# Kernel tuning notes

Measured on AMD Instinct MI355X. Metric: run time of the kernel, lower is better.

Reference implementation:

```python
import jax, jax.numpy as jnp
import numpy as np

HEADS = 8
LANDMARKS = 256
PINV_ITERS = 6
CONV_K = 33


def _layernorm(x, g, b, eps=1e-5):
    mu = x.mean(-1, keepdims=True)
    var = x.var(-1, keepdims=True)
    return (x - mu) * jax.lax.rsqrt(var + eps) * g + b


def _pinv(x, iters=PINV_ITERS):
    # Moore-Penrose iterative pseudo-inverse (lucidrains nystrom-attention)
    ax = jnp.abs(x)
    denom = ax.sum(-1).max() * ax.sum(-2).max()  # global max, as in torch.max()
    z = jnp.swapaxes(x, -1, -2) / denom
    I = jnp.eye(x.shape[-1], dtype=x.dtype)
    for _ in range(iters):
        xz = x @ z
        z = 0.25 * z @ (13 * I - xz @ (15 * I - xz @ (7 * I - xz)))
    return z


def _nystrom_attn(x, qkv_w, out_w, out_b, conv_w):
    b, n, dim = x.shape
    h, m = HEADS, LANDMARKS
    dh = dim // h
    pad = (-n) % m  # pad at the FRONT so n divisible by num_landmarks
    xp = jnp.pad(x, ((0, 0), (pad, 0), (0, 0)))
    npad = n + pad
    qkv = xp @ qkv_w  # [b, npad, 3*dim]
    q, k, v = jnp.split(qkv, 3, axis=-1)

    def to_heads(t):
        return t.reshape(b, npad, h, dh).transpose(0, 2, 1, 3)  # [b,h,npad,dh]

    q, k, v = to_heads(q), to_heads(k), to_heads(v)
    q = q * (dh ** -0.5)
    l = npad // m  # tokens per landmark
    q_l = q.reshape(b, h, m, l, dh).mean(3)  # landmark means [b,h,m,dh]
    k_l = k.reshape(b, h, m, l, dh).mean(3)
    a1 = jax.nn.softmax(jnp.einsum('bhid,bhjd->bhij', q, k_l), axis=-1)   # [b,h,npad,m]
    a2 = jax.nn.softmax(jnp.einsum('bhid,bhjd->bhij', q_l, k_l), axis=-1)  # [b,h,m,m]
    a3 = jax.nn.softmax(jnp.einsum('bhid,bhjd->bhij', q_l, k), axis=-1)   # [b,h,m,npad]
    out = (a1 @ _pinv(a2)) @ (a3 @ v)  # [b,h,npad,dh]
    # residual depthwise conv over sequence dim, one channel per head (bias=False)
    res = jax.lax.conv_general_dilated(
        v, conv_w, window_strides=(1, 1),
        padding=((CONV_K // 2, CONV_K // 2), (0, 0)),
        dimension_numbers=('NCHW', 'OIHW', 'NCHW'),
        feature_group_count=HEADS)
    out = out + res
    out = out.transpose(0, 2, 1, 3).reshape(b, npad, dim)
    out = out @ out_w + out_b
    return out[:, -n:]  # drop front padding


def setup_inputs():
    key = jax.random.key(0)
    ks = jax.random.split(key, 16)
    D_IN, D, C = 1024, 512, 2
    return {
        'feats': jax.random.normal(ks[0], (2, 8000, D_IN), jnp.float32),
        'fc1_w': jax.random.normal(ks[1], (D_IN, D), jnp.float32) * 0.02,
        'fc1_b': jnp.zeros((D,), jnp.float32),
        'cls_token': jax.random.normal(ks[2], (1, 1, D), jnp.float32),
        'ln1_g': jnp.ones((D,), jnp.float32),
        'ln1_b': jnp.zeros((D,), jnp.float32),
        'qkv1_w': jax.random.normal(ks[3], (D, 3 * D), jnp.float32) * 0.02,
        'out1_w': jax.random.normal(ks[4], (D, D), jnp.float32) * 0.02,
        'out1_b': jnp.zeros((D,), jnp.float32),
        'conv1_w': jax.random.normal(ks[5], (HEADS, 1, CONV_K, 1), jnp.float32) * 0.02,
        'ln2_g': jnp.ones((D,), jnp.float32),
        'ln2_b': jnp.zeros((D,), jnp.float32),
        'qkv2_w': jax.random.normal(ks[6], (D, 3 * D), jnp.float32) * 0.02,
        'out2_w': jax.random.normal(ks[7], (D, D), jnp.float32) * 0.02,
        'out2_b': jnp.zeros((D,), jnp.float32),
        'conv2_w': jax.random.normal(ks[8], (HEADS, 1, CONV_K, 1), jnp.float32) * 0.02,
        'normf_g': jnp.ones((D,), jnp.float32),
        'normf_b': jnp.zeros((D,), jnp.float32),
        'fc2_w': jax.random.normal(ks[9], (D, C), jnp.float32) * 0.02,
        'fc2_b': jnp.zeros((C,), jnp.float32),
    }


def reference(feats, fc1_w, fc1_b, cls_token, ln1_g, ln1_b, qkv1_w, out1_w, out1_b, conv1_w,
              ln2_g, ln2_b, qkv2_w, out2_w, out2_b, conv2_w, normf_g, normf_b, fc2_w, fc2_b):
    h = jax.nn.relu(feats @ fc1_w + fc1_b)  # [B,N,512]
    B = h.shape[0]
    cls = jnp.broadcast_to(cls_token, (B, 1, cls_token.shape[-1]))
    h = jnp.concatenate([cls, h], axis=1)  # [B,N+1,512]
    h = h + _nystrom_attn(_layernorm(h, ln1_g, ln1_b), qkv1_w, out1_w, out1_b, conv1_w)
    h = h + _nystrom_attn(_layernorm(h, ln2_g, ln2_b), qkv2_w, out2_w, out2_b, conv2_w)
    h_cls = _layernorm(h, normf_g, normf_b)[:, 0]
    logits = h_cls @ fc2_w + fc2_b
    y_prob = jax.nn.softmax(logits, axis=1)
    y_hat = jnp.argmax(logits, axis=1)
    return logits, y_prob, y_hat
```

## Files before the change

kernel.cpp:

```cpp
#include <hip/hip_runtime.h>

typedef unsigned short u16;
typedef __attribute__((ext_vector_type(8))) short short8;
typedef __attribute__((ext_vector_type(4))) float f32x4;

__device__ __forceinline__ float bf2f(u16 x){
  union { unsigned u; float f; } c; c.u = ((unsigned)x) << 16; return c.f;
}
__device__ __forceinline__ u16 f2bf(float f){
  union { float f; unsigned u; } c; c.f = f;
  unsigned u = c.u;
  return (u16)((u + 0x7FFFu + ((u >> 16) & 1u)) >> 16);
}
__device__ __forceinline__ unsigned pk2(float a, float b){
  return (unsigned)f2bf(a) | ((unsigned)f2bf(b) << 16);
}
__device__ __forceinline__ void hilo(float v, u16& hi, u16& lo){
  hi = f2bf(v); lo = f2bf(v - bf2f(hi));
}

__device__ __forceinline__ void gload16(const void* g, void* l){
  __builtin_amdgcn_global_load_lds(
    (const __attribute__((address_space(1))) void*)g,
    (__attribute__((address_space(3))) void*)l, 16, 0, 0);
}

__global__ void k_cls(const float* cls, float* h){
  int b = blockIdx.x, t = threadIdx.x;
  for (int c=t; c<512; c+=256)
    h[((long)b*8192+191)*512 + c] = cls[c];
}

__global__ void k_cvtT(const float* Wm, u16* wT, int K, int N){
  __shared__ float tile[32][33];
  int n0 = blockIdx.x*32, k0 = blockIdx.y*32;
  int x = threadIdx.x & 31, y = threadIdx.x >> 5;
  #pragma unroll
  for (int p=0;p<4;p++) tile[y+8*p][x] = Wm[(long)(k0+y+8*p)*N + n0 + x];
  __syncthreads();
  #pragma unroll
  for (int p=0;p<4;p++) wT[(long)(n0+y+8*p)*K + k0 + x] = f2bf(tile[x][y+8*p]);
}

template<int MODE>
__launch_bounds__(256)
__global__ void k_gemm(const void* Av, const u16* Bt, const float* bias,
                       float* hout, u16* qo, u16* ko, u16* vo,
                       int M, int N, int K){
  __shared__ __align__(16) u16 As[128*32];
  __shared__ __align__(16) u16 Bs[128*32];
  const int tid = threadIdx.x;
  const int wave = tid>>6, lane = tid&63;
  const int m0 = blockIdx.x*128, n0 = blockIdx.y*128;
  const int wr = wave>>1, wc = wave&1;
  f32x4 acc[4][4];
  #pragma unroll
  for (int i=0;i<4;i++)
    #pragma unroll
    for (int j=0;j<4;j++) acc[i][j] = (f32x4){0.f,0.f,0.f,0.f};

  for (int k0=0; k0<K; k0+=32){
    if constexpr (MODE == 0){
      int r = tid>>1, half = tid&1;
      const float* gp = (const float*)Av + (long)(m0+r)*K + k0 + half*16;
      float4 f0 = *(const float4*)(gp+0);
      float4 f1 = *(const float4*)(gp+4);
      float4 f2 = *(const float4*)(gp+8);
      float4 f3 = *(const float4*)(gp+12);
      uint4 pa, pb;
      pa.x = pk2(f0.x,f0.y); pa.y = pk2(f0.z,f0.w);
      pa.z = pk2(f1.x,f1.y); pa.w = pk2(f1.z,f1.w);
      pb.x = pk2(f2.x,f2.y); pb.y = pk2(f2.z,f2.w);
      pb.z = pk2(f3.x,f3.y); pb.w = pk2(f3.z,f3.w);
      uint4* dst = (uint4*)&As[r*32 + half*16];
      dst[0] = pa; dst[1] = pb;
    } else {
      #pragma unroll
      for (int ci=0; ci<2; ++ci){
        int c = wave*2 + ci;
        int r = (c<<4) + (lane>>2), kq = lane&3;
        const u16* gp;
        if constexpr (MODE == 1){
          gp = (const u16*)Av + (long)(m0+r)*K + k0 + kq*8;
        } else {
          int rr = m0 + r; int b = rr>>13, pos = rr&8191;
          int cc = k0 + kq*8; int hh = cc>>6, d = cc&63;
          gp = (const u16*)Av + ((long)(b*8+hh)*8192 + pos)*64 + d;
        }
        gload16(gp, &As[c*512]);
      }
    }
    #pragma unroll
    for (int ci=0; ci<2; ++ci){
      int c = wave*2 + ci;
      int r = (c<<4) + (lane>>2), kq = lane&3;
      gload16(Bt + (long)(n0+r)*K + k0 + kq*8, &Bs[c*512]);
    }
    __syncthreads();
    short8 af[4], bf[4];
    int arow = wr*64 + (lane&15);
    int brow = wc*64 + (lane&15);
    int koff = (lane>>4)*8;
    #pragma unroll
    for (int i=0;i<4;i++){
      af[i] = *(const short8*)&As[(arow + i*16)*32 + koff];
      bf[i] = *(const short8*)&Bs[(brow + i*16)*32 + koff];
    }
    #pragma unroll
    for (int i=0;i<4;i++)
      #pragma unroll
      for (int j=0;j<4;j++)
        acc[i][j] = __builtin_amdgcn_mfma_f32_16x16x32_bf16(bf[j], af[i], acc[i][j], 0,0,0);
    __syncthreads();
  }

  const int lc = lane&15, hi4 = (lane>>4)*4;
  if constexpr (MODE == 0){
    #pragma unroll
    for (int j=0;j<4;j++){
      int cb = n0 + wc*64 + j*16 + hi4;
      float4 bb = *(const float4*)&bias[cb];
      #pragma unroll
      for (int i=0;i<4;i++){
        int row = m0 + wr*64 + i*16 + lc;
        int b = (row >= 8000) ? 1 : 0;
        int tok = row - b*8000;
        float4 o;
        o.x = fmaxf(acc[i][j][0] + bb.x, 0.f);
        o.y = fmaxf(acc[i][j][1] + bb.y, 0.f);
        o.z = fmaxf(acc[i][j][2] + bb.z, 0.f);
        o.w = fmaxf(acc[i][j][3] + bb.w, 0.f);
        *(float4*)&hout[((long)(b*8192 + 192 + tok))*512 + cb] = o;
      }
    }
  } else if constexpr (MODE == 1){
    #pragma unroll
    for (int j=0;j<4;j++){
      int cb = n0 + wc*64 + j*16 + hi4;
      int which = cb>>9, head = (cb>>6)&7, d = cb&63;
      u16* base = (which==0) ? qo : (which==1 ? ko : vo);
      float scale = (which==0) ? 0.125f : 1.0f;
      #pragma unroll
      for (int i=0;i<4;i++){
        int row = m0 + wr*64 + i*16 + lc;
        int b = row>>13, pos = row&8191;
        unsigned o2[2];
        o2[0] = pk2(acc[i][j][0]*scale, acc[i][j][1]*scale);
        o2[1] = pk2(acc[i][j][2]*scale, acc[i][j][3]*scale);
        *(uint2*)&base[((long)(b*8+head)*8192 + pos)*64 + d] = *(uint2*)o2;
      }
    }
  } else {
    #pragma unroll
    for (int j=0;j<4;j++){
      int cb = n0 + wc*64 + j*16 + hi4;
      float4 bb = *(const float4*)&bias[cb];
      #pragma unroll
      for (int i=0;i<4;i++){
        int row = m0 + wr*64 + i*16 + lc;
        int pos = row&8191;
        if (pos < 191) continue;
        float4* p = (float4*)&hout[(long)row*512 + cb];
        float4 cur = *p;
        cur.x += acc[i][j][0] + bb.x;
        cur.y += acc[i][j][1] + bb.y;
        cur.z += acc[i][j][2] + bb.z;
        cur.w += acc[i][j][3] + bb.w;
        *p = cur;
      }
    }
  }
}

__global__ void k_ln(const float* hsrc, const float* g, const float* bt, u16* xlnb){
  int row = blockIdx.x;
  int pos = row & 8191;
  int t = threadIdx.x;
  long base = (long)row*512 + t*2;
  if (pos < 191){ *(unsigned*)&xlnb[base] = 0u; return; }
  float2 x = *(const float2*)(hsrc + base);
  __shared__ float red[4];
  float s = x.x + x.y;
  for (int off=32; off; off>>=1) s += __shfl_down(s, off, 64);
  if ((t&63)==0) red[t>>6]=s;
  __syncthreads();
  float mean = (red[0]+red[1]+red[2]+red[3]) * (1.f/512.f);
  __syncthreads();
  float d0 = x.x-mean, d1 = x.y-mean;
  float ss = d0*d0 + d1*d1;
  for (int off=32; off; off>>=1) ss += __shfl_down(ss, off, 64);
  if ((t&63)==0) red[t>>6]=ss;
  __syncthreads();
  float rstd = rsqrtf((red[0]+red[1]+red[2]+red[3])*(1.f/512.f) + 1e-5f);
  float o0 = d0*rstd*g[t*2]   + bt[t*2];
  float o1 = d1*rstd*g[t*2+1] + bt[t*2+1];
  *(unsigned*)&xlnb[base] = pk2(o0, o1);
}

__global__ void k_landmark(const u16* src, float* dst, u16* dstb){
  int g = blockIdx.x, bh = blockIdx.y, d = threadIdx.x;
  const u16* p = src + (((long)bh*8192) + g*32)*64 + d;
  float s = 0.f;
  #pragma unroll
  for (int j=0;j<32;j++) s += bf2f(p[j*64]);
  s *= (1.f/32.f);
  long o = ((long)bh*256 + g)*64 + d;
  dst[o] = s;
  dstb[o] = f2bf(s);
}

__launch_bounds__(256)
__global__ void k_a2(const float* qlm, const float* klm, float* a2, u16* a2Nh, u16* a2Nl){
  __shared__ float qls[16][68];
  __shared__ float kls[64][65];
  __shared__ float Sf[16][260];
  __shared__ float red[4];
  int bh = blockIdx.y, rt = blockIdx.x, t = threadIdx.x;
  const float* qp = qlm + ((long)bh*256 + rt*16)*64;
  { int fidx = t*4; int r = fidx>>6, c = fidx&63;
    float4 a = *(const float4*)(qp + fidx);
    qls[r][c]=a.x; qls[r][c+1]=a.y; qls[r][c+2]=a.z; qls[r][c+3]=a.w; }
  const float* kp = klm + (long)bh*16384;
  int cl = t & 63, ig = t >> 6;
  for (int kt=0; kt<4; ++kt){
    __syncthreads();
    for (int l=0;l<4;l++){
      int fidx = (l*256+t)*4; int r = fidx>>6, c = fidx&63;
      float4 a = *(const float4*)(kp + (long)(kt*64+r)*64 + c);
      kls[r][c]=a.x; kls[r][c+1]=a.y; kls[r][c+2]=a.z; kls[r][c+3]=a.w;
    }
    __syncthreads();
    float s0=0,s1=0,s2=0,s3=0;
    #pragma unroll
    for (int d=0;d<64;d++){
      float kv = kls[cl][d];
      s0 += qls[ig*4+0][d]*kv;
      s1 += qls[ig*4+1][d]*kv;
      s2 += qls[ig*4+2][d]*kv;
      s3 += qls[ig*4+3][d]*kv;
    }
    Sf[ig*4+0][kt*64+cl]=s0;
    Sf[ig*4+1][kt*64+cl]=s1;
    Sf[ig*4+2][kt*64+cl]=s2;
    Sf[ig*4+3][kt*64+cl]=s3;
  }
  __syncthreads();
  long ab = ((long)bh*256 + rt*16)*256;
  for (int i=0;i<16;i++){
    float val = Sf[i][t];
    float m = val;
    for (int off=1; off<64; off<<=1) m = fmaxf(m, __shfl_xor(m,off,64));
    if ((t&63)==0) red[t>>6]=m;
    __syncthreads();
    m = fmaxf(fmaxf(red[0],red[1]),fmaxf(red[2],red[3]));
    __syncthreads();
    float e = __expf(val - m);
    float sum = e;
    for (int off=1; off<64; off<<=1) sum += __shfl_xor(sum,off,64);
    if ((t&63)==0) red[t>>6]=sum;
    __syncthreads();
    sum = red[0]+red[1]+red[2]+red[3];
    __syncthreads();
    float o = e/sum;
    long idx = ab + (long)i*256 + t;
    a2[idx] = o;
    u16 hi, lo; hilo(o, hi, lo);
    a2Nh[idx]=hi; a2Nl[idx]=lo;
  }
}

__global__ void k_colrow(const float* a2, float* rc){
  int bh = blockIdx.x, t = threadIdx.x;
  const float* p = a2 + (long)bh*65536;
  float cs=0.f, rs=0.f;
  for (int r=0;r<256;r++) cs += fabsf(p[(long)r*256 + t]);
  for (int c=0;c<256;c++) rs += fabsf(p[(long)t*256 + c]);
  __shared__ float red[4];
  for (int off=32; off; off>>=1) cs = fmaxf(cs, __shfl_down(cs,off,64));
  if ((t&63)==0) red[t>>6]=cs;
  __syncthreads();
  if (t==0) rc[bh] = fmaxf(fmaxf(red[0],red[1]),fmaxf(red[2],red[3]));
  __syncthreads();
  for (int off=32; off; off>>=1) rs = fmaxf(rs, __shfl_down(rs,off,64));
  if ((t&63)==0) red[t>>6]=rs;
  __syncthreads();
  if (t==0) rc[16+bh] = fmaxf(fmaxf(red[0],red[1]),fmaxf(red[2],red[3]));
}
__global__ void k_denom(const float* rc, float* denom){
  float cm=0.f, rm=0.f;
  for (int i=0;i<16;i++){ cm=fmaxf(cm,rc[i]); rm=fmaxf(rm,rc[16+i]); }
  *denom = cm*rm;
}

__global__ void k_z0p(const float* a2, const float* denom,
                      u16* zNh, u16* zNl, u16* zTh, u16* zTl){
  __shared__ float tile[32][33];
  int bh = blockIdx.z;
  int c0 = blockIdx.x*32, r0 = blockIdx.y*32;
  int x = threadIdx.x & 31, y = threadIdx.x >> 5;
  const float* p = a2 + (long)bh*65536;
  float inv = 1.0f / (*denom);
  long zb = (long)bh*65536;
  #pragma unroll
  for (int yy=0; yy<32; yy+=8){
    float vv = p[(long)(r0+y+yy)*256 + c0 + x];
    tile[y+yy][x] = vv;
    float val = vv*inv;
    u16 hi, lo; hilo(val, hi, lo);
    long idx = zb + (long)(r0+y+yy)*256 + c0 + x;
    zTh[idx]=hi; zTl[idx]=lo;
  }
  __syncthreads();
  #pragma unroll
  for (int yy=0; yy<32; yy+=8){
    float val = tile[x][y+yy]*inv;
    u16 hi, lo; hilo(val, hi, lo);
    long idx = zb + (long)(c0+y+yy)*256 + r0 + x;
    zNh[idx]=hi; zNl[idx]=lo;
  }
}

struct NC {
  const u16 *Ah, *Al, *Bh, *Bl;
  const u16 *E1h, *E1l, *E2h, *E2l;
  u16 *oNh, *oNl, *oTh, *oTl, *oBF;
  long strA, strB, strO;
  float sa, s1, s2;
};

__launch_bounds__(64)
__global__ void k_nmm(NC c0, NC c1){
  int gz = blockIdx.z;
  int bh = gz & 15;
  NC C = (gz>>4) ? c1 : c0;
  __shared__ __align__(16) char smem[8192];
  u16* AsH = (u16*)smem;
  u16* AsL = (u16*)(smem + 2048);
  u16* BsH = (u16*)(smem + 4096);
  u16* BsL = (u16*)(smem + 6144);
  float* T = (float*)smem;
  int lane = threadIdx.x;
  int m0 = blockIdx.x*32, n0 = blockIdx.y*32;
  int lc = lane&15, hi = lane>>4;
  f32x4 acc[2][2];
  #pragma unroll
  for (int i=0;i<2;i++)
    #pragma unroll
    for (int j=0;j<2;j++) acc[i][j] = (f32x4){0.f,0.f,0.f,0.f};

  const u16* pAh = C.Ah + (long)bh*C.strA;
  const u16* pAl = C.Al + (long)bh*C.strA;
  const u16* pBh = C.Bh + (long)bh*C.strB;
  const u16* pBl = C.Bl + (long)bh*C.strB;
  int r0 = lane>>2, kq = lane&3;
  int r1 = r0 + 16;
  long offA0 = (long)(m0+r0)*256 + ((kq ^ ((r0>>1)&3))<<3);
  long offA1 = (long)(m0+r1)*256 + ((kq ^ ((r1>>1)&3))<<3);
  long offB0 = (long)(n0+r0)*256 + ((kq ^ ((r0>>1)&3))<<3);
  long offB1 = (long)(n0+r1)*256 + ((kq ^ ((r1>>1)&3))<<3);

  for (int k0=0; k0<256; k0+=32){
    gload16(pAh + offA0 + k0, smem + 0);
    gload16(pAh + offA1 + k0, smem + 1024);
    gload16(pAl + offA0 + k0, smem + 2048);
    gload16(pAl + offA1 + k0, smem + 3072);
    gload16(pBh + offB0 + k0, smem + 4096);
    gload16(pBh + offB1 + k0, smem + 5120);
    gload16(pBl + offB0 + k0, smem + 6144);
    gload16(pBl + offB1 + k0, smem + 7168);
    __syncthreads();
    short8 aH[2], aL[2], bH[2], bL[2];
    #pragma unroll
    for (int i=0;i<2;i++){
      int ra = i*16 + lc;
      int ca = ((hi ^ ((ra>>1)&3)))<<3;
      aH[i] = *(const short8*)&AsH[ra*32 + ca];
      aL[i] = *(const short8*)&AsL[ra*32 + ca];
      bH[i] = *(const short8*)&BsH[ra*32 + ca];
      bL[i] = *(const short8*)&BsL[ra*32 + ca];
    }
    #pragma unroll
    for (int i=0;i<2;i++)
      #pragma unroll
      for (int j=0;j<2;j++){
        acc[i][j] = __builtin_amdgcn_mfma_f32_16x16x32_bf16(aH[i], bH[j], acc[i][j], 0,0,0);
        acc[i][j] = __builtin_amdgcn_mfma_f32_16x16x32_bf16(aH[i], bL[j], acc[i][j], 0,0,0);
        acc[i][j] = __builtin_amdgcn_mfma_f32_16x16x32_bf16(aL[i], bH[j], acc[i][j], 0,0,0);
      }
    __syncthreads();
  }

  long eb = (long)bh*65536;
  #pragma unroll
  for (int i=0;i<2;i++)
    #pragma unroll
    for (int j=0;j<2;j++){
      int rg = i*16 + hi*4;
      int cg = j*16 + lc;
      #pragma unroll
      for (int r=0;r<4;r++){
        float val = C.sa*acc[i][j][r];
        long ei = eb + (long)(m0+rg+r)*256 + (n0+cg);
        if (C.E1h) val += C.s1*(bf2f(C.E1h[ei]) + bf2f(C.E1l[ei]));
        if (C.E2h) val += C.s2*(bf2f(C.E2h[ei]) + bf2f(C.E2l[ei]));
        T[(rg+r)*34 + cg] = val;
      }
    }
  __syncthreads();
  int rr = lane>>1, cc0 = (lane&1)*16;
  if (C.oBF){
    u16 tmp[16];
    #pragma unroll
    for (int m=0;m<16;m++) tmp[m] = f2bf(T[rr*34 + cc0 + m]);
    long ob = (long)bh*C.strO + (long)(m0+rr)*256 + n0 + cc0;
    *(uint4*)&C.oBF[ob]   = *(uint4*)&tmp[0];
    *(uint4*)&C.oBF[ob+8] = *(uint4*)&tmp[8];
  } else {
    u16 th[16], tl[16];
    #pragma unroll
    for (int m=0;m<16;m++) hilo(T[rr*34 + cc0 + m], th[m], tl[m]);
    long ob = (long)bh*65536 + (long)(m0+rr)*256 + n0 + cc0;
    *(uint4*)&C.oNh[ob]   = *(uint4*)&th[0];
    *(uint4*)&C.oNh[ob+8] = *(uint4*)&th[8];
    *(uint4*)&C.oNl[ob]   = *(uint4*)&tl[0];
    *(uint4*)&C.oNl[ob+8] = *(uint4*)&tl[8];
    if (C.oTh){
      #pragma unroll
      for (int m=0;m<16;m++) hilo(T[(cc0+m)*34 + rr], th[m], tl[m]);
      long obt = (long)bh*65536 + (long)(n0+rr)*256 + m0 + cc0;
      *(uint4*)&C.oTh[obt]   = *(uint4*)&th[0];
      *(uint4*)&C.oTh[obt+8] = *(uint4*)&th[8];
      *(uint4*)&C.oTl[obt]   = *(uint4*)&tl[0];
      *(uint4*)&C.oTl[obt+8] = *(uint4*)&tl[8];
    }
  }
}

__launch_bounds__(256)
__global__ void k_vt(const u16* v, u16* vt){
  __shared__ u16 tile[32][80];
  int pt = blockIdx.x, bh = blockIdx.y, t = threadIdx.x;
  int p = t>>3, d0 = (t&7)*8;
  *(uint4*)&tile[p][d0] = *(const uint4*)(v + ((long)bh*8192 + pt*32 + p)*64 + d0);
  __syncthreads();
  int d = t>>2, seg = t&3;
  u16 tmp[8];
  #pragma unroll
  for (int j=0;j<8;j++) tmp[j] = tile[seg*8+j][d];
  *(uint4*)&vt[((long)(bh*64 + d))*8192 + pt*32 + seg*8] = *(uint4*)tmp;
}

template<int OM>
__launch_bounds__(256)
__global__ void k_flash2(const u16* Q, const u16* K, const u16* VT,
                         float* op, float* ml, u16* hb,
                         int kvchunk, long qbh, long kbh, long vtbh, int vtrow){
  __shared__ __align__(16) u16 KT[64*64];
  __shared__ __align__(16) u16 VTs[64*64];
  __shared__ __align__(16) u16 Pb[4*16*72];
  int bh = blockIdx.y, qt = blockIdx.x, sk = (OM==0) ? blockIdx.z : 0;
  int t = threadIdx.x, w = t>>6, l = t&63;
  int lq = l&15, hi = l>>4;

  short8 qf[2];
  {
    const u16* qp = Q + (long)bh*qbh + (long)(qt*64 + w*16 + lq)*64 + hi*8;
    qf[0] = *(const short8*)(qp);
    qf[1] = *(const short8*)(qp + 32);
  }
  float m_run = -1e30f, l_run = 0.f;
  f32x4 o[4];
  #pragma unroll
  for (int i=0;i<4;i++) o[i] = (f32x4){0.f,0.f,0.f,0.f};

  const u16* kbase = K + (long)bh*kbh;
  const u16* vtbase = VT + (long)bh*vtbh;
  char* Pw = (char*)&Pb[w*16*72];
  int kv0 = sk*kvchunk;

  for (int p0 = kv0; p0 < kv0 + kvchunk; p0 += 64){
    #pragma unroll
    for (int ii=0; ii<2; ++ii){
      int inst = w*2 + ii;
      int r = inst*8 + (l>>3);
      int ch = l&7;
      gload16(kbase + (long)(p0+r)*64 + ((ch ^ (r&7))<<3), (char*)KT + inst*1024);
    }
    #pragma unroll
    for (int ii=0; ii<2; ++ii){
      int inst = w*2 + ii;
      int d = inst*8 + (l>>3);
      int srcoff = ((l&7)*16) ^ ((d&7)<<4);
      const char* src = (const char*)(vtbase + (long)d*vtrow + p0) + srcoff;
      gload16(src, (char*)VTs + inst*1024);
    }
    __syncthreads();
    f32x4 s[4];
    #pragma unroll
    for (int i=0;i<4;i++){
      s[i] = (f32x4){0.f,0.f,0.f,0.f};
      #pragma unroll
      for (int kh=0;kh<2;kh++){
        int kvr = i*16 + lq;
        int byte = (kvr*128 + hi*16 + kh*64) ^ ((kvr&7)<<4);
        short8 kf = *(const short8*)((const char*)KT + byte);
        s[i] = __builtin_amdgcn_mfma_f32_16x16x32_bf16(kf, qf[kh], s[i], 0,0,0);
      }
    }
    float tm = -1e30f;
    #pragma unroll
    for (int i=0;i<4;i++)
      #pragma unroll
      for (int r=0;r<4;r++) tm = fmaxf(tm, s[i][r]);
    tm = fmaxf(tm, __shfl_xor(tm, 16));
    tm = fmaxf(tm, __shfl_xor(tm, 32));
    float mnew = fmaxf(m_run, tm);
    float scale = __expf(m_run - mnew);
    float tsum = 0.f;
    #pragma unroll
    for (int i=0;i<4;i++)
      #pragma unroll
      for (int r=0;r<4;r++){ float e = __expf(s[i][r]-mnew); s[i][r]=e; tsum += e; }
    tsum += __shfl_xor(tsum, 16);
    tsum += __shfl_xor(tsum, 32);
    l_run = l_run*scale + tsum;
    m_run = mnew;
    #pragma unroll
    for (int i=0;i<4;i++)
      #pragma unroll
      for (int r=0;r<4;r++) o[i][r] *= scale;
    #pragma unroll
    for (int i=0;i<4;i++){
      int byte = lq*144 + (i*16 + hi*4)*2;
      *(unsigned*)(Pw + byte)     = pk2(s[i][0], s[i][1]);
      *(unsigned*)(Pw + byte + 4) = pk2(s[i][2], s[i][3]);
    }
    short8 pf[2];
    #pragma unroll
    for (int kh=0;kh<2;kh++)
      pf[kh] = *(const short8*)(Pw + lq*144 + hi*16 + kh*64);
    #pragma unroll
    for (int i=0;i<4;i++){
      #pragma unroll
      for (int kh=0;kh<2;kh++){
        int d = i*16 + lq;
        int byte = (d*128 + hi*16 + kh*64) ^ ((d&7)<<4);
        short8 vf = *(const short8*)((const char*)VTs + byte);
        o[i] = __builtin_amdgcn_mfma_f32_16x16x32_bf16(vf, pf[kh], o[i], 0,0,0);
      }
    }
    __syncthreads();
  }

  int qrow = qt*64 + w*16 + lq;
  if constexpr (OM == 0){
    long ob = ((long)(sk*16+bh)*256 + qrow)*64;
    #pragma unroll
    for (int i=0;i<4;i++)
      #pragma unroll
      for (int r=0;r<4;r++) op[ob + i*16 + hi*4 + r] = o[i][r];
    if (l < 16){
      long mi = ((long)(sk*16+bh)*256 + qt*64 + w*16 + l)*2;
      ml[mi] = m_run; ml[mi+1] = l_run;
    }
  } else {
    float invl = 1.f/l_run;
    long hb0 = ((long)bh*8192 + qrow)*64;
    #pragma unroll
    for (int i=0;i<4;i++)
      #pragma unroll
      for (int r=0;r<4;r++){
        long idx = hb0 + i*16 + hi*4 + r;
        hb[idx] = f2bf(bf2f(hb[idx]) + o[i][r]*invl);
      }
  }
}

__global__ void k_fcomb(const float* op, const float* ml, u16* w3Th, u16* w3Tl){
  int bh = blockIdx.y, rt = blockIdx.x, t = threadIdx.x;
  int row = rt*16 + (t>>4), d0 = (t&15)*4;
  float M = -1e30f;
  for (int s=0;s<16;s++) M = fmaxf(M, ml[(((long)(s*16+bh)*256)+row)*2]);
  float lt = 0.f;
  float4 o = {0,0,0,0};
  for (int s=0;s<16;s++){
    long base = ((long)(s*16+bh)*256)+row;
    float w = __expf(ml[base*2]-M);
    lt += ml[base*2+1]*w;
    float4 ov = *(const float4*)&op[base*64 + d0];
    o.x += ov.x*w; o.y += ov.y*w; o.z += ov.z*w; o.w += ov.w*w;
  }
  float inv = 1.f/lt;
  float vals[4] = {o.x*inv, o.y*inv, o.z*inv, o.w*inv};
  #pragma unroll
  for (int dd=0; dd<4; ++dd){
    u16 hi, lo; hilo(vals[dd], hi, lo);
    long idx = (long)bh*32768 + (long)(d0+dd)*256 + row;
    w3Th[idx]=hi; w3Tl[idx]=lo;
  }
}

__launch_bounds__(256)
__global__ void k_conv(const u16* v, const float* cw, u16* heads){
  __shared__ float vsl[160][64];
  __shared__ float cws[33];
  int bh = blockIdx.y, pt = blockIdx.x, t = threadIdx.x;
  int hh = bh & 7;
  if (t < 33) cws[t] = cw[hh*33 + t];
  int p0 = pt*128;
  const u16* vp = v + (long)bh*8192*64;
  for (int l=0;l<5;l++){
    int fidx = (l*256 + t)*8;
    int r = fidx>>6, c = fidx&63;
    int gp = p0 - 16 + r;
    if (gp>=0 && gp<8192){
      uint4 a = *(const uint4*)(vp + (long)gp*64 + c);
      const u16* pp = (const u16*)&a;
      #pragma unroll
      for (int m=0;m<8;m++) vsl[r][c+m] = bf2f(pp[m]);
    } else {
      #pragma unroll
      for (int m=0;m<8;m++) vsl[r][c+m] = 0.f;
    }
  }
  __syncthreads();
  int d = t & 63, pg = t >> 6;
  u16* hp = heads + ((long)bh*8192 + p0)*64;
  for (int pp=0; pp<32; pp++){
    int pl = pp*4 + pg;
    float acc = 0.f;
    #pragma unroll
    for (int tt=0; tt<33; tt++) acc += vsl[pl+tt][d]*cws[tt];
    hp[(long)pl*64 + d] = f2bf(acc);
  }
}

__global__ void k_final(const float* hbuf, const float* g, const float* bt,
                        const float* fw, const float* fb, float* outp){
  int b = blockIdx.x, t = threadIdx.x;
  __shared__ float red[4];
  __shared__ float sx[512];
  __shared__ float lg[4];
  const float* x = hbuf + ((long)b*8192+191)*512;
  float2 xv = *(const float2*)(x + t*2);
  float s = xv.x + xv.y;
  for (int off=32; off; off>>=1) s += __shfl_down(s,off,64);
  if ((t&63)==0) red[t>>6]=s;
  __syncthreads();
  float mean = (red[0]+red[1]+red[2]+red[3])*(1.f/512.f);
  __syncthreads();
  float d0 = xv.x-mean, d1 = xv.y-mean;
  float ssq = d0*d0 + d1*d1;
  for (int off=32; off; off>>=1) ssq += __shfl_down(ssq,off,64);
  if ((t&63)==0) red[t>>6]=ssq;
  __syncthreads();
  float rstd = rsqrtf((red[0]+red[1]+red[2]+red[3])*(1.f/512.f) + 1e-5f);
  sx[t*2]   = d0*rstd*g[t*2]   + bt[t*2];
  sx[t*2+1] = d1*rstd*g[t*2+1] + bt[t*2+1];
  __syncthreads();
  int c = t>>7, jj = t&127;
  float part = 0.f;
  for (int kk=jj; kk<512; kk+=128) part += sx[kk]*fw[(long)kk*2 + c];
  for (int off=1; off<64; off<<=1) part += __shfl_xor(part,off,64);
  if ((t&63)==0) lg[t>>6]=part;
  __syncthreads();
  if (t==0){
    float l0 = lg[0]+lg[1] + fb[0];
    float l1 = lg[2]+lg[3] + fb[1];
    float m = fmaxf(l0,l1);
    float e0 = __expf(l0-m), e1 = __expf(l1-m);
    float inv = 1.f/(e0+e1);
    outp[b*2+0]=l0; outp[b*2+1]=l1;
    outp[4+b*2+0]=e0*inv; outp[4+b*2+1]=e1*inv;
    outp[8+b]=(l1>l0) ? 1.f : 0.f;
  }
}

static NC mkc(const u16* Ah,const u16* Al,const u16* Bh,const u16* Bl,
              const u16* E1h,const u16* E1l,const u16* E2h,const u16* E2l,
              u16* oNh,u16* oNl,u16* oTh,u16* oTl,u16* oBF,
              long strA,long strB,long strO,float sa,float s1,float s2){
  NC c; c.Ah=Ah;c.Al=Al;c.Bh=Bh;c.Bl=Bl;c.E1h=E1h;c.E1l=E1l;c.E2h=E2h;c.E2l=E2l;
  c.oNh=oNh;c.oNl=oNl;c.oTh=oTh;c.oTl=oTl;c.oBF=oBF;
  c.strA=strA;c.strB=strB;c.strO=strO;c.sa=sa;c.s1=s1;c.s2=s2; return c;
}

extern "C" void kernel_launch(void* const* d_in, const int* in_sizes, int n_in,
                              void* d_out, int out_size, void* d_ws, size_t ws_size,
                              hipStream_t stream){
  (void)in_sizes; (void)n_in; (void)out_size; (void)ws_size;
  const long TOK = (long)2*8192*512;
  const long PL = 1048576;
  float* W    = (float*)d_ws;
  float* rc   = W;
  float* h    = W + 64;
  u16*  q     = (u16*)(h + TOK);
  u16*  k     = q + TOK;
  u16*  v     = k + TOK;
  u16*  xlnb  = v + TOK;
  u16*  zPl   = xlnb;
  u16*  headsb= xlnb + TOK;
  u16*  wT    = headsb + TOK;
  float* ql   = (float*)(wT + PL);
  float* kl   = ql + 262144;
  u16*  qlb   = (u16*)(kl + 262144);
  u16*  klb   = qlb + 262144;
  float* a2f  = (float*)(klb + 262144);
  u16*  a2Nh  = (u16*)(a2f + 1048576);
  u16*  a2Nl  = a2Nh + PL;
  u16*  YNh   = a2Nl + PL;
  u16*  YNl   = YNh + PL;
  u16*  YTh   = YNl + PL;
  u16*  YTl   = YTh + PL;
  u16*  Gth   = YTl + PL;
  u16*  Gtl   = Gth + PL;
  u16*  PNh   = Gtl + PL;
  u16*  PNl   = PNh + PL;
  u16*  PTh   = PNl + PL;
  u16*  PTl   = PTh + PL;
  u16*  w3Th  = PTl + PL;
  u16*  w3Tl  = w3Th + 524288;
  u16*  zwT   = w3Tl + 524288;
  u16*  vt    = zwT + 262144;
  float* op   = (float*)v;
  float* ml   = a2f;

  u16* zN_h[2] = { zPl,        zPl + 4*PL };
  u16* zN_l[2] = { zPl + PL,   zPl + 5*PL };
  u16* zT_h[2] = { zPl + 2*PL, zPl + 6*PL };
  u16* zT_l[2] = { zPl + 3*PL, zPl + 7*PL };

  dim3 B(256);

  k_cls<<<dim3(2), B, 0, stream>>>((const float*)d_in[3], h);
  k_cvtT<<<dim3(16,32), B, 0, stream>>>((const float*)d_in[1], wT, 1024, 512);
  k_gemm<0><<<dim3(125,4), B, 0, stream>>>(d_in[0], wT, (const float*)d_in[2],
                                           h, nullptr,nullptr,nullptr, 16000,512,1024);

  for (int blk=0; blk<2; ++blk){
    const float* lng  = (const float*)d_in[blk?10:4];
    const float* lnb  = (const float*)d_in[blk?11:5];
    const float* qkvw = (const float*)d_in[blk?12:6];
    const float* outw = (const float*)d_in[blk?13:7];
    const float* outb = (const float*)d_in[blk?14:8];
    const float* cw   = (const float*)d_in[blk?15:9];

    k_ln<<<dim3(16384), B, 0, stream>>>(h, lng, lnb, xlnb);

    k_cvtT<<<dim3(48,16), B, 0, stream>>>(qkvw, wT, 512, 1536);
    k_gemm<1><<<dim3(128,12), B, 0, stream>>>(xlnb, wT, nullptr,
                                              nullptr, q,k,v, 16384,1536,512);

    k_landmark<<<dim3(256,16), dim3(64), 0, stream>>>(q, ql, qlb);
    k_landmark<<<dim3(256,16), dim3(64), 0, stream>>>(k, kl, klb);

    k_vt<<<dim3(256,16), B, 0, stream>>>(v, vt);
    k_conv<<<dim3(64,16), B, 0, stream>>>(v, cw, headsb);

    k_a2<<<dim3(16,16), B, 0, stream>>>(ql, kl, a2f, a2Nh, a2Nl);
    k_colrow<<<dim3(16), B, 0, stream>>>(a2f, rc);
    k_denom<<<dim3(1), dim3(1), 0, stream>>>(rc, rc+32);
    k_z0p<<<dim3(8,8,16), B, 0, stream>>>(a2f, rc+32, zN_h[0],zN_l[0],zT_h[0],zT_l[0]);

    for (int it=0; it<6; ++it){
      int zi = it&1, zo = (it+1)&1;
      NC s1 = mkc(a2Nh,a2Nl, zT_h[zi],zT_l[zi], nullptr,nullptr,nullptr,nullptr,
                  YNh,YNl, YTh,YTl, nullptr, 65536,65536,0, 1.f,0.f,0.f);
      k_nmm<<<dim3(8,8,16), dim3(64), 0, stream>>>(s1, s1);
      NC s2a = mkc(YTh,YTl, YNh,YNl, YTh,YTl, nullptr,nullptr,
                   Gth,Gtl, nullptr,nullptr, nullptr, 65536,65536,0, -1.f,7.f,0.f);
      NC s2b = mkc(zN_h[zi],zN_l[zi], YTh,YTl, nullptr,nullptr,nullptr,nullptr,
                   PNh,PNl, PTh,PTl, nullptr, 65536,65536,0, 1.f,0.f,0.f);
      k_nmm<<<dim3(8,8,32), dim3(64), 0, stream>>>(s2a, s2b);
      NC s3 = mkc(PNh,PNl, Gth,Gtl, zN_h[zi],zN_l[zi], PNh,PNl,
                  zN_h[zo],zN_l[zo], zT_h[zo],zT_l[zo], nullptr,
                  65536,65536,0, 0.25f,3.25f,-3.75f);
      k_nmm<<<dim3(8,8,16), dim3(64), 0, stream>>>(s3, s3);
    }

    k_flash2<0><<<dim3(4,16,16), B, 0, stream>>>(qlb, k, vt, op, ml, nullptr,
                                                 512, 16384L, 524288L, 524288L, 8192);
    k_fcomb<<<dim3(16,16), B, 0, stream>>>(op, ml, w3Th, w3Tl);
    NC zwc = mkc(w3Th,w3Tl, zN_h[0],zN_l[0], nullptr,nullptr,nullptr,nullptr,
                 nullptr,nullptr,nullptr,nullptr, zwT, 32768,65536,16384, 1.f,0.f,0.f);
    k_nmm<<<dim3(2,8,16), dim3(64), 0, stream>>>(zwc, zwc);
    k_flash2<1><<<dim3(128,16,1), B, 0, stream>>>(q, klb, zwT, nullptr, nullptr, headsb,
                                                  256, 524288L, 16384L, 16384L, 256);

    k_cvtT<<<dim3(16,16), B, 0, stream>>>(outw, wT, 512, 512);
    k_gemm<2><<<dim3(128,4), B, 0, stream>>>(headsb, wT, outb,
                                             h, nullptr,nullptr,nullptr, 16384,512,512);
  }

  k_final<<<dim3(2), B, 0, stream>>>(h, (const float*)d_in[16], (const float*)d_in[17],
                                     (const float*)d_in[18], (const float*)d_in[19], (float*)d_out);
}
```

Measured before the change: 1.205 ms.

## Fuse Newton-Schulz pinv iterations into one persistent kernel with grid barriers

Replaces the 18 per-iteration k_nmm launches plus the final z·w3 launch with a single persistent kernel of 256 blocks. Each block owns a 64x64 tile, built from four waves per block instead of one-wave 32x32 tiles. Phases are separated by an atomic global barrier whose counter is reset in k_colrow. This removes per-launch overhead and tail effects on the serial chain of small matmuls. In exchange it relies on all 256 blocks being co-resident and uses fewer, larger blocks per GEMM phase.

After: 2.441 ms. 103% more time.

```diff
diff --git a/kernel.cpp b/kernel.cpp
--- a/kernel.cpp
+++ b/kernel.cpp
@@ -269,8 +269,9 @@
   }
 }
 
-__global__ void k_colrow(const float* a2, float* rc){
+__global__ void k_colrow(const float* a2, float* rc, int* bar){
   int bh = blockIdx.x, t = threadIdx.x;
+  if (bh==0 && t==0) *bar = 0;
   const float* p = a2 + (long)bh*65536;
   float cs=0.f, rs=0.f;
   for (int r=0;r<256;r++) cs += fabsf(p[(long)r*256 + t]);
@@ -320,27 +321,23 @@
   }
 }
 
-struct NC {
-  const u16 *Ah, *Al, *Bh, *Bl;
-  const u16 *E1h, *E1l, *E2h, *E2l;
-  u16 *oNh, *oNl, *oTh, *oTl, *oBF;
-  long strA, strB, strO;
-  float sa, s1, s2;
+struct PC {
+  const u16 *Ah,*Al,*Bh,*Bl;
+  const u16 *E1h,*E1l,*E2h,*E2l;
+  u16 *oNh,*oNl,*oTh,*oTl,*oBF;
+  long strA,strB,strO;
+  float sa,s1,s2;
 };
 
-__launch_bounds__(64)
-__global__ void k_nmm(NC c0, NC c1){
-  int gz = blockIdx.z;
-  int bh = gz & 15;
-  NC C = (gz>>4) ? c1 : c0;
-  __shared__ __align__(16) char smem[8192];
+__device__ __forceinline__ void nmm64(const PC& C, int bh, int m0, int n0,
+                                      char* smem, int tid){
   u16* AsH = (u16*)smem;
-  u16* AsL = (u16*)(smem + 2048);
-  u16* BsH = (u16*)(smem + 4096);
-  u16* BsL = (u16*)(smem + 6144);
+  u16* AsL = (u16*)(smem + 4096);
+  u16* BsH = (u16*)(smem + 8192);
+  u16* BsL = (u16*)(smem + 12288);
   float* T = (float*)smem;
-  int lane = threadIdx.x;
-  int m0 = blockIdx.x*32, n0 = blockIdx.y*32;
+  int wave = tid>>6, lane = tid&63;
+  int wr = wave>>1, wc = wave&1;
   int lc = lane&15, hi = lane>>4;
   f32x4 acc[2][2];
   #pragma unroll
@@ -348,36 +345,32 @@
     #pragma unroll
     for (int j=0;j<2;j++) acc[i][j] = (f32x4){0.f,0.f,0.f,0.f};
 
-  const u16* pAh = C.Ah + (long)bh*C.strA;
-  const u16* pAl = C.Al + (long)bh*C.strA;
-  const u16* pBh = C.Bh + (long)bh*C.strB;
-  const u16* pBl = C.Bl + (long)bh*C.strB;
-  int r0 = lane>>2, kq = lane&3;
-  int r1 = r0 + 16;
-  long offA0 = (long)(m0+r0)*256 + ((kq ^ ((r0>>1)&3))<<3);
-  long offA1 = (long)(m0+r1)*256 + ((kq ^ ((r1>>1)&3))<<3);
-  long offB0 = (long)(n0+r0)*256 + ((kq ^ ((r0>>1)&3))<<3);
-  long offB1 = (long)(n0+r1)*256 + ((kq ^ ((r1>>1)&3))<<3);
+  const u16* plane = (wave==0) ? C.Ah : (wave==1) ? C.Al : (wave==2) ? C.Bh : C.Bl;
+  long pstr = (wave<2) ? C.strA : C.strB;
+  int rbase = (wave<2) ? m0 : n0;
+  const u16* pb = plane + (long)bh*pstr;
+  char* dstbase = smem + wave*4096;
+  int srow = lane>>2, skq = lane&3;
 
   for (int k0=0; k0<256; k0+=32){
-    gload16(pAh + offA0 + k0, smem + 0);
-    gload16(pAh + offA1 + k0, smem + 1024);
-    gload16(pAl + offA0 + k0, smem + 2048);
-    gload16(pAl + offA1 + k0, smem + 3072);
-    gload16(pBh + offB0 + k0, smem + 4096);
-    gload16(pBh + offB1 + k0, smem + 5120);
-    gload16(pBl + offB0 + k0, smem + 6144);
-    gload16(pBl + offB1 + k0, smem + 7168);
+    #pragma unroll
+    for (int ii=0; ii<4; ++ii){
+      int row = ii*16 + srow;
+      int kcs = k0 + ((skq ^ ((row>>1)&3))<<3);
+      gload16(pb + (long)(rbase+row)*256 + kcs, dstbase + ii*1024);
+    }
     __syncthreads();
     short8 aH[2], aL[2], bH[2], bL[2];
     #pragma unroll
     for (int i=0;i<2;i++){
-      int ra = i*16 + lc;
-      int ca = ((hi ^ ((ra>>1)&3)))<<3;
+      int ra = wr*32 + i*16 + lc;
+      int ca = ((hi ^ ((ra>>1)&3)))*8;
       aH[i] = *(const short8*)&AsH[ra*32 + ca];
       aL[i] = *(const short8*)&AsL[ra*32 + ca];
-      bH[i] = *(const short8*)&BsH[ra*32 + ca];
-      bL[i] = *(const short8*)&BsL[ra*32 + ca];
+      int rb = wc*32 + i*16 + lc;
+      int cb = ((hi ^ ((rb>>1)&3)))*8;
+      bH[i] = *(const short8*)&BsH[rb*32 + cb];
+      bL[i] = *(const short8*)&BsL[rb*32 + cb];
     }
     #pragma unroll
     for (int i=0;i<2;i++)
@@ -395,30 +388,30 @@
   for (int i=0;i<2;i++)
     #pragma unroll
     for (int j=0;j<2;j++){
-      int rg = i*16 + hi*4;
-      int cg = j*16 + lc;
+      int rg = wr*32 + i*16 + hi*4;
+      int cg = wc*32 + j*16 + lc;
       #pragma unroll
       for (int r=0;r<4;r++){
         float val = C.sa*acc[i][j][r];
         long ei = eb + (long)(m0+rg+r)*256 + (n0+cg);
         if (C.E1h) val += C.s1*(bf2f(C.E1h[ei]) + bf2f(C.E1l[ei]));
         if (C.E2h) val += C.s2*(bf2f(C.E2h[ei]) + bf2f(C.E2l[ei]));
-        T[(rg+r)*34 + cg] = val;
+        T[(rg+r)*68 + cg] = val;
       }
     }
   __syncthreads();
-  int rr = lane>>1, cc0 = (lane&1)*16;
+  int rr = tid>>2, cc0 = (tid&3)*16;
   if (C.oBF){
     u16 tmp[16];
     #pragma unroll
-    for (int m=0;m<16;m++) tmp[m] = f2bf(T[rr*34 + cc0 + m]);
+    for (int m=0;m<16;m++) tmp[m] = f2bf(T[rr*68 + cc0 + m]);
     long ob = (long)bh*C.strO + (long)(m0+rr)*256 + n0 + cc0;
     *(uint4*)&C.oBF[ob]   = *(uint4*)&tmp[0];
     *(uint4*)&C.oBF[ob+8] = *(uint4*)&tmp[8];
   } else {
     u16 th[16], tl[16];
     #pragma unroll
-    for (int m=0;m<16;m++) hilo(T[rr*34 + cc0 + m], th[m], tl[m]);
+    for (int m=0;m<16;m++) hilo(T[rr*68 + cc0 + m], th[m], tl[m]);
     long ob = (long)bh*65536 + (long)(m0+rr)*256 + n0 + cc0;
     *(uint4*)&C.oNh[ob]   = *(uint4*)&th[0];
     *(uint4*)&C.oNh[ob+8] = *(uint4*)&th[8];
@@ -426,13 +419,73 @@
     *(uint4*)&C.oNl[ob+8] = *(uint4*)&tl[8];
     if (C.oTh){
       #pragma unroll
-      for (int m=0;m<16;m++) hilo(T[(cc0+m)*34 + rr], th[m], tl[m]);
+      for (int m=0;m<16;m++) hilo(T[(cc0+m)*68 + rr], th[m], tl[m]);
       long obt = (long)bh*65536 + (long)(n0+rr)*256 + m0 + cc0;
       *(uint4*)&C.oTh[obt]   = *(uint4*)&th[0];
       *(uint4*)&C.oTh[obt+8] = *(uint4*)&th[8];
       *(uint4*)&C.oTl[obt]   = *(uint4*)&tl[0];
       *(uint4*)&C.oTl[obt+8] = *(uint4*)&tl[8];
     }
+  }
+  __syncthreads();
+}
+
+__device__ __forceinline__ void gbar(int* bar, int need){
+  __syncthreads();
+  if (threadIdx.x == 0){
+    __threadfence();
+    __hip_atomic_fetch_add(bar, 1, __ATOMIC_ACQ_REL, __HIP_MEMORY_SCOPE_AGENT);
+    while (__hip_atomic_load(bar, __ATOMIC_ACQUIRE, __HIP_MEMORY_SCOPE_AGENT) < need)
+      __builtin_amdgcn_s_sleep(1);
+    __threadfence();
+  }
+  __syncthreads();
+}
+
+__launch_bounds__(256)
+__global__ void k_newton(const u16* a2Nh, const u16* a2Nl,
+                         u16* zNh0,u16* zNl0,u16* zTh0,u16* zTl0,
+                         u16* zNh1,u16* zNl1,u16* zTh1,u16* zTl1,
+                         u16* YNh,u16* YNl,u16* YTh,u16* YTl,
+                         u16* Gth,u16* Gtl,
+                         u16* PNh,u16* PNl,u16* PTh,u16* PTl,
+                         const u16* w3Th,const u16* w3Tl,u16* zwT,
+                         int* bar){
+  __shared__ __align__(16) char smem[64*68*4];
+  const int tid = threadIdx.x;
+  const int b = blockIdx.x;
+  const int bh = b>>4, tile = b&15;
+  const int m0 = (tile>>2)*64, n0 = (tile&3)*64;
+  u16 *ziNh=zNh0,*ziNl=zNl0,*ziTh=zTh0,*ziTl=zTl0;
+  u16 *zoNh=zNh1,*zoNl=zNl1,*zoTh=zTh1,*zoTl=zTl1;
+  int ph = 0;
+  #pragma unroll 1
+  for (int it=0; it<6; ++it){
+    PC s1{a2Nh,a2Nl, ziTh,ziTl, nullptr,nullptr,nullptr,nullptr,
+          YNh,YNl, YTh,YTl, nullptr, 65536L,65536L,0L, 1.f,0.f,0.f};
+    nmm64(s1, bh, m0, n0, smem, tid);
+    ++ph; gbar(bar, ph*256);
+    PC s2a{YTh,YTl, YNh,YNl, YTh,YTl, nullptr,nullptr,
+           Gth,Gtl, nullptr,nullptr, nullptr, 65536L,65536L,0L, -1.f,7.f,0.f};
+    nmm64(s2a, bh, m0, n0, smem, tid);
+    PC s2b{ziNh,ziNl, YTh,YTl, nullptr,nullptr,nullptr,nullptr,
+           PNh,PNl, PTh,PTl, nullptr, 65536L,65536L,0L, 1.f,0.f,0.f};
+    nmm64(s2b, bh, m0, n0, smem, tid);
+    ++ph; gbar(bar, ph*256);
+    PC s3{PNh,PNl, Gth,Gtl, ziNh,ziNl, PNh,PNl,
+          zoNh,zoNl, zoTh,zoTl, nullptr, 65536L,65536L,0L, 0.25f,3.25f,-3.75f};
+    nmm64(s3, bh, m0, n0, smem, tid);
+    ++ph; gbar(bar, ph*256);
+    u16* t;
+    t=ziNh; ziNh=zoNh; zoNh=t;
+    t=ziNl; ziNl=zoNl; zoNl=t;
+    t=ziTh; ziTh=zoTh; zoTh=t;
+    t=ziTl; ziTl=zoTl; zoTl=t;
+  }
+  if (m0 == 0){
+    PC zw{w3Th,w3Tl, ziNh,ziNl, nullptr,nullptr,nullptr,nullptr,
+          nullptr,nullptr,nullptr,nullptr, zwT, 32768L,65536L,16384L, 1.f,0.f,0.f};
+    nmm64(zw, bh, 0, n0, smem, tid);
   }
 }
 
@@ -676,15 +729,6 @@
   }
 }
 
-static NC mkc(const u16* Ah,const u16* Al,const u16* Bh,const u16* Bl,
-              const u16* E1h,const u16* E1l,const u16* E2h,const u16* E2l,
-              u16* oNh,u16* oNl,u16* oTh,u16* oTl,u16* oBF,
-              long strA,long strB,long strO,float sa,float s1,float s2){
-  NC c; c.Ah=Ah;c.Al=Al;c.Bh=Bh;c.Bl=Bl;c.E1h=E1h;c.E1l=E1l;c.E2h=E2h;c.E2l=E2l;
-  c.oNh=oNh;c.oNl=oNl;c.oTh=oTh;c.oTl=oTl;c.oBF=oBF;
-  c.strA=strA;c.strB=strB;c.strO=strO;c.sa=sa;c.s1=s1;c.s2=s2; return c;
-}
-
 extern "C" void kernel_launch(void* const* d_in, const int* in_sizes, int n_in,
                               void* d_out, int out_size, void* d_ws, size_t ws_size,
                               hipStream_t stream){
@@ -693,6 +737,7 @@
   const long PL = 1048576;
   float* W    = (float*)d_ws;
   float* rc   = W;
+  int*  bar   = (int*)(W + 48);
   float* h    = W + 64;
   u16*  q     = (u16*)(h + TOK);
   u16*  k     = q + TOK;
@@ -758,32 +803,21 @@
     k_conv<<<dim3(64,16), B, 0, stream>>>(v, cw, headsb);
 
     k_a2<<<dim3(16,16), B, 0, stream>>>(ql, kl, a2f, a2Nh, a2Nl);
-    k_colrow<<<dim3(16), B, 0, stream>>>(a2f, rc);
+    k_colrow<<<dim3(16), B, 0, stream>>>(a2f, rc, bar);
     k_denom<<<dim3(1), dim3(1), 0, stream>>>(rc, rc+32);
     k_z0p<<<dim3(8,8,16), B, 0, stream>>>(a2f, rc+32, zN_h[0],zN_l[0],zT_h[0],zT_l[0]);
-
-    for (int it=0; it<6; ++it){
-      int zi = it&1, zo = (it+1)&1;
-      NC s1 = mkc(a2Nh,a2Nl, zT_h[zi],zT_l[zi], nullptr,nullptr,nullptr,nullptr,
-                  YNh,YNl, YTh,YTl, nullptr, 65536,65536,0, 1.f,0.f,0.f);
-      k_nmm<<<dim3(8,8,16), dim3(64), 0, stream>>>(s1, s1);
-      NC s2a = mkc(YTh,YTl, YNh,YNl, YTh,YTl, nullptr,nullptr,
-                   Gth,Gtl, nullptr,nullptr, nullptr, 65536,65536,0, -1.f,7.f,0.f);
-      NC s2b = mkc(zN_h[zi],zN_l[zi], YTh,YTl, nullptr,nullptr,nullptr,nullptr,
-                   PNh,PNl, PTh,PTl, nullptr, 65536,65536,0, 1.f,0.f,0.f);
-      k_nmm<<<dim3(8,8,32), dim3(64), 0, stream>>>(s2a, s2b);
-      NC s3 = mkc(PNh,PNl, Gth,Gtl, zN_h[zi],zN_l[zi], PNh,PNl,
-                  zN_h[zo],zN_l[zo], zT_h[zo],zT_l[zo], nullptr,
-                  65536,65536,0, 0.25f,3.25f,-3.75f);
-      k_nmm<<<dim3(8,8,16), dim3(64), 0, stream>>>(s3, s3);
-    }
 
     k_flash2<0><<<dim3(4,16,16), B, 0, stream>>>(qlb, k, vt, op, ml, nullptr,
                                                  512, 16384L, 524288L, 524288L, 8192);
     k_fcomb<<<dim3(16,16), B, 0, stream>>>(op, ml, w3Th, w3Tl);
-    NC zwc = mkc(w3Th,w3Tl, zN_h[0],zN_l[0], nullptr,nullptr,nullptr,nullptr,
-                 nullptr,nullptr,nullptr,nullptr, zwT, 32768,65536,16384, 1.f,0.f,0.f);
-    k_nmm<<<dim3(2,8,16), dim3(64), 0, stream>>>(zwc, zwc);
+
+    k_newton<<<dim3(256), B, 0, stream>>>(a2Nh,a2Nl,
+                                          zN_h[0],zN_l[0],zT_h[0],zT_l[0],
+                                          zN_h[1],zN_l[1],zT_h[1],zT_l[1],
+                                          YNh,YNl,YTh,YTl, Gth,Gtl,
+                                          PNh,PNl,PTh,PTl,
+                                          w3Th,w3Tl, zwT, bar);
+
     k_flash2<1><<<dim3(128,16,1), B, 0, stream>>>(q, klb, zwT, nullptr, nullptr, headsb,
                                                   256, 524288L, 16384L, 16384L, 256);
 
```
